# Optimization experiments

Hardware: AMD Instinct MI355X
Metric: run time of the kernel (lower is better)

The kernel has to match this reference:

```python
import jax, jax.numpy as jnp
import numpy as np

N_CHANNELS = 8
SECTION = 32768
F_IN = 64
F_OUT = 64
UNITS = 512


def setup_inputs() -> dict:
    key = jax.random.key(0)
    ks = jax.random.split(key, 10)
    scale = lambda fan_in: 1.0 / np.sqrt(fan_in)
    return {
        "x": jax.random.normal(ks[0], (N_CHANNELS * SECTION, F_IN), jnp.float32),
        "w0": jax.random.normal(ks[1], (N_CHANNELS, UNITS, F_IN), jnp.float32) * scale(F_IN),
        "w1": jax.random.normal(ks[2], (N_CHANNELS, UNITS, UNITS), jnp.float32) * scale(UNITS),
        "w2": jax.random.normal(ks[3], (N_CHANNELS, UNITS, UNITS), jnp.float32) * scale(UNITS),
        "w3": jax.random.normal(ks[4], (N_CHANNELS, F_OUT, UNITS), jnp.float32) * scale(UNITS),
        "b0": jax.random.normal(ks[5], (N_CHANNELS, UNITS), jnp.float32) * 0.01,
        "b1": jax.random.normal(ks[6], (N_CHANNELS, UNITS), jnp.float32) * 0.01,
        "b2": jax.random.normal(ks[7], (N_CHANNELS, UNITS), jnp.float32) * 0.01,
        "b3": jax.random.normal(ks[8], (N_CHANNELS, F_OUT), jnp.float32) * 0.01,
        "section_size": SECTION,
    }


def reference(x, w0, w1, w2, w3, b0, b1, b2, b3, section_size):
    # Equal sections of size `section_size` per channel: reshape to [C, S, F]
    # and run the per-channel MLP as batched (grouped) GEMMs.
    C = w0.shape[0]
    xs = x.reshape(C, section_size, -1)  # [C, S, F_in]
    for w, b in ((w0, b0), (w1, b1), (w2, b2)):
        xs = jax.nn.relu(jnp.einsum('csi,coi->cso', xs, w) + b[:, None, :])
    ys = jnp.einsum('csi,coi->cso', xs, w3) + b3[:, None, :]  # [C, S, F_out]
    return ys.reshape(C * section_size, -1)
```

## Files before the change

### kernel.cpp

```cpp
#include <hip/hip_runtime.h>
#include <hip/hip_bf16.h>

#define CH 8
#define SEC 32768
#define FIN 64
#define FOUT 64
#define UN 512
#define BM 64

typedef __bf16 bf16;
typedef bf16 bf16x8 __attribute__((ext_vector_type(8)));
typedef bf16 bf16x4 __attribute__((ext_vector_type(4)));
typedef float f32x4 __attribute__((ext_vector_type(4)));

__device__ __forceinline__ bf16x8 cvt8(const float* __restrict__ src) {
  f32x4 u0 = *(const f32x4*)src;
  f32x4 u1 = *(const f32x4*)(src + 4);
  bf16x8 v;
  v[0] = (bf16)u0[0]; v[1] = (bf16)u0[1]; v[2] = (bf16)u0[2]; v[3] = (bf16)u0[3];
  v[4] = (bf16)u1[0]; v[5] = (bf16)u1[1]; v[6] = (bf16)u1[2]; v[7] = (bf16)u1[3];
  return v;
}

__device__ __forceinline__ void store_cvt8(void* dst, const float* __restrict__ src) {
  *(bf16x8*)dst = cvt8(src);
}

template<int K, bool WSPATH>
__device__ __forceinline__ void run_main_layer(
    const bf16* __restrict__ wb,
    const float* __restrict__ wf,
    const float* __restrict__ bias, char* __restrict__ act,
    int w, int l, int l15, int l4, int rot)
{
  constexpr int NKS = K / 32;
  constexpr int MASK = NKS - 1;
  const int col0 = w * 64;
  const char* abase = act + l * 16;

  f32x4 acc[4][4];
#pragma unroll
  for (int mt = 0; mt < 4; ++mt)
#pragma unroll
    for (int nt = 0; nt < 4; ++nt)
      acc[mt][nt] = f32x4{0.f, 0.f, 0.f, 0.f};

  if constexpr (WSPATH) {
    const bf16* bp = wb + ((size_t)(w * 4) * NKS * 64 + l) * 8;

    bf16x8 B0[4], B1[4];
    {
      const int ks0 = rot & MASK;
#pragma unroll
      for (int i = 0; i < 4; ++i)
        B0[i] = *(const bf16x8*)(bp + ((size_t)i * NKS + ks0) * 512);
    }

#pragma unroll
    for (int j = 0; j < NKS; j += 2) {
      {
        const int ksn = (j + 1 + rot) & MASK;
#pragma unroll
        for (int i = 0; i < 4; ++i)
          B1[i] = *(const bf16x8*)(bp + ((size_t)i * NKS + ksn) * 512);
        const int ks = (j + rot) & MASK;
        bf16x8 a[4];
#pragma unroll
        for (int mt = 0; mt < 4; ++mt)
          a[mt] = *(const bf16x8*)(abase + (mt * NKS + ks) * 1024);
        __builtin_amdgcn_s_setprio(1);
#pragma unroll
        for (int mt = 0; mt < 4; ++mt)
#pragma unroll
          for (int nt = 0; nt < 4; ++nt)
            acc[mt][nt] = __builtin_amdgcn_mfma_f32_16x16x32_bf16(a[mt], B0[nt], acc[mt][nt], 0, 0, 0);
        __builtin_amdgcn_s_setprio(0);
      }
      {
        if (j + 2 < NKS) {
          const int ksn = (j + 2 + rot) & MASK;
#pragma unroll
          for (int i = 0; i < 4; ++i)
            B0[i] = *(const bf16x8*)(bp + ((size_t)i * NKS + ksn) * 512);
        }
        const int ks = (j + 1 + rot) & MASK;
        bf16x8 a[4];
#pragma unroll
        for (int mt = 0; mt < 4; ++mt)
          a[mt] = *(const bf16x8*)(abase + (mt * NKS + ks) * 1024);
        __builtin_amdgcn_s_setprio(1);
#pragma unroll
        for (int mt = 0; mt < 4; ++mt)
#pragma unroll
          for (int nt = 0; nt < 4; ++nt)
            acc[mt][nt] = __builtin_amdgcn_mfma_f32_16x16x32_bf16(a[mt], B1[nt], acc[mt][nt], 0, 0, 0);
        __builtin_amdgcn_s_setprio(0);
      }
    }
  } else {
    const float* bpf[4];
#pragma unroll
    for (int nt = 0; nt < 4; ++nt)
      bpf[nt] = wf + (size_t)(col0 + nt * 16 + l15) * K + l4 * 8;
    for (int j = 0; j < NKS; ++j) {
      const int ks = (j + rot) & MASK;
      bf16x8 a[4], b[4];
#pragma unroll
      for (int nt = 0; nt < 4; ++nt) b[nt] = cvt8(bpf[nt] + ks * 32);
#pragma unroll
      for (int mt = 0; mt < 4; ++mt)
        a[mt] = *(const bf16x8*)(abase + (mt * NKS + ks) * 1024);
#pragma unroll
      for (int mt = 0; mt < 4; ++mt)
#pragma unroll
        for (int nt = 0; nt < 4; ++nt)
          acc[mt][nt] = __builtin_amdgcn_mfma_f32_16x16x32_bf16(a[mt], b[nt], acc[mt][nt], 0, 0, 0);
    }
  }

  __syncthreads();

#pragma unroll
  for (int nt = 0; nt < 4; ++nt) {
    const int col = col0 + nt * 16 + l15;
    const float bv = bias[col];
    const int base = (col >> 5) * 1024 + ((col >> 3) & 3) * 256 + (col & 7) * 2 + l4 * 64;
#pragma unroll
    for (int mt = 0; mt < 4; ++mt)
#pragma unroll
      for (int r = 0; r < 4; ++r) {
        float v = acc[mt][nt][r] + bv;
        v = v > 0.f ? v : 0.f;
        *(bf16*)(act + mt * 16384 + base + r * 16) = (bf16)v;
      }
  }
  __syncthreads();
}

template<bool WSPATH>
__device__ __forceinline__ void run_final_layer(
    const bf16* __restrict__ wb, const float* __restrict__ wf,
    const float* __restrict__ bias, const char* __restrict__ act,
    float* __restrict__ gout,
    int w, int l, int l15, int l4, int rot)
{
  constexpr int NKS = 16;
  const int mt = w >> 1;
  const int nb = (w & 1) * 2;
  const char* abase = act + mt * 16384 + l * 16;

  f32x4 acc[2];
  acc[0] = f32x4{0.f, 0.f, 0.f, 0.f};
  acc[1] = f32x4{0.f, 0.f, 0.f, 0.f};

  if constexpr (WSPATH) {
    const bf16* bp0 = wb + ((size_t)(nb + 0) * 16 * 64 + l) * 8;
    const bf16* bp1 = wb + ((size_t)(nb + 1) * 16 * 64 + l) * 8;
    bf16x8 B0[2], B1[2];
    B0[0] = *(const bf16x8*)(bp0 + (size_t)(rot & 15) * 512);
    B0[1] = *(const bf16x8*)(bp1 + (size_t)(rot & 15) * 512);
#pragma unroll
    for (int j = 0; j < NKS; j += 2) {
      {
        const int ksn = (j + 1 + rot) & 15;
        B1[0] = *(const bf16x8*)(bp0 + (size_t)ksn * 512);
        B1[1] = *(const bf16x8*)(bp1 + (size_t)ksn * 512);
        const int ks = (j + rot) & 15;
        const bf16x8 a = *(const bf16x8*)(abase + ks * 1024);
        acc[0] = __builtin_amdgcn_mfma_f32_16x16x32_bf16(a, B0[0], acc[0], 0, 0, 0);
        acc[1] = __builtin_amdgcn_mfma_f32_16x16x32_bf16(a, B0[1], acc[1], 0, 0, 0);
      }
      {
        if (j + 2 < NKS) {
          const int ksn = (j + 2 + rot) & 15;
          B0[0] = *(const bf16x8*)(bp0 + (size_t)ksn * 512);
          B0[1] = *(const bf16x8*)(bp1 + (size_t)ksn * 512);
        }
        const int ks = (j + 1 + rot) & 15;
        const bf16x8 a = *(const bf16x8*)(abase + ks * 1024);
        acc[0] = __builtin_amdgcn_mfma_f32_16x16x32_bf16(a, B1[0], acc[0], 0, 0, 0);
        acc[1] = __builtin_amdgcn_mfma_f32_16x16x32_bf16(a, B1[1], acc[1], 0, 0, 0);
      }
    }
  } else {
    const float* bpf0 = wf + (size_t)((nb + 0) * 16 + l15) * UN + l4 * 8;
    const float* bpf1 = wf + (size_t)((nb + 1) * 16 + l15) * UN + l4 * 8;
    for (int j = 0; j < NKS; ++j) {
      const int ks = (j + rot) & 15;
      const bf16x8 b0 = cvt8(bpf0 + ks * 32);
      const bf16x8 b1 = cvt8(bpf1 + ks * 32);
      const bf16x8 a = *(const bf16x8*)(abase + ks * 1024);
      acc[0] = __builtin_amdgcn_mfma_f32_16x16x32_bf16(a, b0, acc[0], 0, 0, 0);
      acc[1] = __builtin_amdgcn_mfma_f32_16x16x32_bf16(a, b1, acc[1], 0, 0, 0);
    }
  }

#pragma unroll
  for (int i = 0; i < 2; ++i) {
    const int col = (nb + i) * 16 + l15;
    const float bv = bias[col];
#pragma unroll
    for (int r = 0; r < 4; ++r)
      gout[(size_t)(mt * 16 + l4 * 4 + r) * FOUT + col] = acc[i][r] + bv;
  }
}

template<bool WSPATH>
__global__ __launch_bounds__(512, 2) void mlp_fused(
    const float* __restrict__ x,
    const float* __restrict__ w0f, const float* __restrict__ w1f,
    const float* __restrict__ w2f, const float* __restrict__ w3f,
    const float* __restrict__ b0, const float* __restrict__ b1,
    const float* __restrict__ b2, const float* __restrict__ b3,
    const bf16* __restrict__ wbase,
    float* __restrict__ out)
{
  extern __shared__ char smem[];
  char* act = smem;

  const int tid = threadIdx.x;
  const int w = tid >> 6, l = tid & 63;
  const int l15 = l & 15, l4 = l >> 4;

  const int wg = (blockIdx.x & 7) * 512 + (blockIdx.x >> 3);
  const int ch = wg >> 9;
  const int row0 = (wg & 511) * BM;
  const int rot = wg & 15;

  const bf16* w0b = wbase + (size_t)ch * UN * FIN;
  const bf16* w1b = wbase + CH * UN * FIN + (size_t)ch * UN * UN;
  const bf16* w2b = wbase + CH * UN * FIN + CH * UN * UN + (size_t)ch * UN * UN;
  const bf16* w3b = wbase + CH * UN * FIN + 2 * CH * UN * UN + (size_t)ch * FOUT * UN;
  const float* w0c = w0f + (size_t)ch * UN * FIN;
  const float* w1c = w1f + (size_t)ch * UN * UN;
  const float* w2c = w2f + (size_t)ch * UN * UN;
  const float* w3c = w3f + (size_t)ch * FOUT * UN;
  const float* b0c = b0 + ch * UN;
  const float* b1c = b1 + ch * UN;
  const float* b2c = b2 + ch * UN;
  const float* b3c = b3 + ch * FOUT;

  {
    const float* xs = x + (size_t)(ch * SEC + row0) * FIN;
    store_cvt8(act + w * 1024 + l * 16,
               xs + ((w >> 1) * 16 + l15) * FIN + (w & 1) * 32 + l4 * 8);
  }
  __syncthreads();

  run_main_layer<64,  WSPATH>(w0b, w0c, b0c, act, w, l, l15, l4, rot);
  run_main_layer<512, WSPATH>(w1b, w1c, b1c, act, w, l, l15, l4, rot);
  run_main_layer<512, WSPATH>(w2b, w2c, b2c, act, w, l, l15, l4, rot);
  run_final_layer<WSPATH>(w3b, w3c, b3c, act,
                          out + (size_t)(ch * SEC + row0) * FOUT,
                          w, l, l15, l4, rot);
}

template<int K, int N>
__device__ __forceinline__ void cvt_one(const float* __restrict__ src,
                                        bf16* __restrict__ dst, int t)
{
  constexpr int NKS = K / 32;
  constexpr int perCh = N * K / 8;
  const int ch = t / perCh;
  const int r = t - ch * perCh;
  const int l = r & 63;
  const int p = r >> 6;
  const int ks = p & (NKS - 1);
  const int f = p / NKS;
  const float* s = src + (size_t)ch * N * K + (size_t)(f * 16 + (l & 15)) * K
                 + ks * 32 + (l >> 4) * 8;
  store_cvt8(dst + (size_t)t * 8, s);
}

__global__ void cvt_weights(const float* __restrict__ w0, const float* __restrict__ w1,
                            const float* __restrict__ w2, const float* __restrict__ w3,
                            bf16* __restrict__ o)
{
  constexpr int T0 = CH * UN * FIN / 8;
  constexpr int T1 = CH * UN * UN / 8;
  constexpr int total = 2 * T0 + 2 * T1;
  for (int t = blockIdx.x * blockDim.x + threadIdx.x; t < total;
       t += gridDim.x * blockDim.x) {
    if (t < T0)                cvt_one<FIN, UN>(w0, o, t);
    else if (t < T0 + T1)      cvt_one<UN, UN>(w1, o + CH * UN * FIN, t - T0);
    else if (t < T0 + 2 * T1)  cvt_one<UN, UN>(w2, o + CH * UN * FIN + CH * UN * UN, t - T0 - T1);
    else                       cvt_one<UN, FOUT>(w3, o + CH * UN * FIN + 2 * CH * UN * UN, t - T0 - 2 * T1);
  }
}

extern "C" void kernel_launch(void* const* d_in, const int* in_sizes, int n_in,
                              void* d_out, int out_size, void* d_ws, size_t ws_size,
                              hipStream_t stream)
{
  const float* x  = (const float*)d_in[0];
  const float* w0 = (const float*)d_in[1];
  const float* w1 = (const float*)d_in[2];
  const float* w2 = (const float*)d_in[3];
  const float* w3 = (const float*)d_in[4];
  const float* b0 = (const float*)d_in[5];
  const float* b1 = (const float*)d_in[6];
  const float* b2 = (const float*)d_in[7];
  const float* b3 = (const float*)d_in[8];
  float* out = (float*)d_out;

  const int grid = CH * (SEC / BM);
  const size_t wbytes = (size_t)(2 * CH * UN * FIN + 2 * CH * UN * UN) * 2;

  if (ws_size >= wbytes) {
    bf16* wb = (bf16*)d_ws;
    hipLaunchKernelGGL(cvt_weights, dim3(2304), dim3(256), 0, stream, w0, w1, w2, w3, wb);
    hipFuncSetAttribute(reinterpret_cast<const void*>(mlp_fused<true>),
                        hipFuncAttributeMaxDynamicSharedMemorySize, 65536);
    hipLaunchKernelGGL(mlp_fused<true>, dim3(grid), dim3(512), 65536, stream,
                       x, w0, w1, w2, w3, b0, b1, b2, b3, wb, out);
  } else {
    hipFuncSetAttribute(reinterpret_cast<const void*>(mlp_fused<false>),
                        hipFuncAttributeMaxDynamicSharedMemorySize, 65536);
    hipLaunchKernelGGL(mlp_fused<false>, dim3(grid), dim3(512), 65536, stream,
                       x, w0, w1, w2, w3, b0, b1, b2, b3, (const bf16*)nullptr, out);
  }
}
```

Measured before the change: 309.5 us.

## Swap MFMA operands to emit transposed tiles with packed bf16x4 stores, drop K rotation

Swaps the A/B operands of every MFMA so each lane holds four consecutive output columns for one row. The epilogue can then load the bias as a float4, pack four bf16 results into one 8-byte LDS store, and write the final fp32 output with 16-byte global stores instead of scalar ones. It also removes the per-workgroup K-start rotation, which makes all loop offsets compile-time constants, and fully unrolls the fallback path. The aim is fewer LDS and global store instructions and simpler addressing. Without the rotation, workgroups on the same channel may read the same weight lines at the same time.

Result: faster. 302.8 us (-2.1%).

```diff
diff --git a/kernel.cpp b/kernel.cpp
--- a/kernel.cpp
+++ b/kernel.cpp
@@ -31,10 +31,9 @@
     const bf16* __restrict__ wb,
     const float* __restrict__ wf,
     const float* __restrict__ bias, char* __restrict__ act,
-    int w, int l, int l15, int l4, int rot)
+    int w, int l, int l15, int l4)
 {
   constexpr int NKS = K / 32;
-  constexpr int MASK = NKS - 1;
   const int col0 = w * 64;
   const char* abase = act + l * 16;
 
@@ -47,53 +46,47 @@
 
   if constexpr (WSPATH) {
     const bf16* bp = wb + ((size_t)(w * 4) * NKS * 64 + l) * 8;
-
     bf16x8 B0[4], B1[4];
-    {
-      const int ks0 = rot & MASK;
-#pragma unroll
-      for (int i = 0; i < 4; ++i)
-        B0[i] = *(const bf16x8*)(bp + ((size_t)i * NKS + ks0) * 512);
-    }
+#pragma unroll
+    for (int i = 0; i < 4; ++i)
+      B0[i] = *(const bf16x8*)(bp + (size_t)(i * NKS) * 512);
 
 #pragma unroll
     for (int j = 0; j < NKS; j += 2) {
+      if (j + 1 < NKS) {
+#pragma unroll
+        for (int i = 0; i < 4; ++i)
+          B1[i] = *(const bf16x8*)(bp + (size_t)(i * NKS + j + 1) * 512);
+      }
       {
-        const int ksn = (j + 1 + rot) & MASK;
+        bf16x8 a[4];
+#pragma unroll
+        for (int mt = 0; mt < 4; ++mt)
+          a[mt] = *(const bf16x8*)(abase + (mt * NKS + j) * 1024);
+        __builtin_amdgcn_s_setprio(1);
+#pragma unroll
+        for (int mt = 0; mt < 4; ++mt)
+#pragma unroll
+          for (int nt = 0; nt < 4; ++nt)
+            acc[mt][nt] = __builtin_amdgcn_mfma_f32_16x16x32_bf16(B0[nt], a[mt], acc[mt][nt], 0, 0, 0);
+        __builtin_amdgcn_s_setprio(0);
+      }
+      if (j + 2 < NKS) {
 #pragma unroll
         for (int i = 0; i < 4; ++i)
-          B1[i] = *(const bf16x8*)(bp + ((size_t)i * NKS + ksn) * 512);
-        const int ks = (j + rot) & MASK;
+          B0[i] = *(const bf16x8*)(bp + (size_t)(i * NKS + j + 2) * 512);
+      }
+      if (j + 1 < NKS) {
         bf16x8 a[4];
 #pragma unroll
         for (int mt = 0; mt < 4; ++mt)
-          a[mt] = *(const bf16x8*)(abase + (mt * NKS + ks) * 1024);
+          a[mt] = *(const bf16x8*)(abase + (mt * NKS + j + 1) * 1024);
         __builtin_amdgcn_s_setprio(1);
 #pragma unroll
         for (int mt = 0; mt < 4; ++mt)
 #pragma unroll
           for (int nt = 0; nt < 4; ++nt)
-            acc[mt][nt] = __builtin_amdgcn_mfma_f32_16x16x32_bf16(a[mt], B0[nt], acc[mt][nt], 0, 0, 0);
-        __builtin_amdgcn_s_setprio(0);
-      }
-      {
-        if (j + 2 < NKS) {
-          const int ksn = (j + 2 + rot) & MASK;
-#pragma unroll
-          for (int i = 0; i < 4; ++i)
-            B0[i] = *(const bf16x8*)(bp + ((size_t)i * NKS + ksn) * 512);
-        }
-        const int ks = (j + 1 + rot) & MASK;
-        bf16x8 a[4];
-#pragma unroll
-        for (int mt = 0; mt < 4; ++mt)
-          a[mt] = *(const bf16x8*)(abase + (mt * NKS + ks) * 1024);
-        __builtin_amdgcn_s_setprio(1);
-#pragma unroll
-        for (int mt = 0; mt < 4; ++mt)
-#pragma unroll
-          for (int nt = 0; nt < 4; ++nt)
-            acc[mt][nt] = __builtin_amdgcn_mfma_f32_16x16x32_bf16(a[mt], B1[nt], acc[mt][nt], 0, 0, 0);
+            acc[mt][nt] = __builtin_amdgcn_mfma_f32_16x16x32_bf16(B1[nt], a[mt], acc[mt][nt], 0, 0, 0);
         __builtin_amdgcn_s_setprio(0);
       }
     }
@@ -102,19 +95,19 @@
 #pragma unroll
     for (int nt = 0; nt < 4; ++nt)
       bpf[nt] = wf + (size_t)(col0 + nt * 16 + l15) * K + l4 * 8;
+#pragma unroll
     for (int j = 0; j < NKS; ++j) {
-      const int ks = (j + rot) & MASK;
       bf16x8 a[4], b[4];
 #pragma unroll
-      for (int nt = 0; nt < 4; ++nt) b[nt] = cvt8(bpf[nt] + ks * 32);
+      for (int nt = 0; nt < 4; ++nt) b[nt] = cvt8(bpf[nt] + j * 32);
 #pragma unroll
       for (int mt = 0; mt < 4; ++mt)
-        a[mt] = *(const bf16x8*)(abase + (mt * NKS + ks) * 1024);
+        a[mt] = *(const bf16x8*)(abase + (mt * NKS + j) * 1024);
 #pragma unroll
       for (int mt = 0; mt < 4; ++mt)
 #pragma unroll
         for (int nt = 0; nt < 4; ++nt)
-          acc[mt][nt] = __builtin_amdgcn_mfma_f32_16x16x32_bf16(a[mt], b[nt], acc[mt][nt], 0, 0, 0);
+          acc[mt][nt] = __builtin_amdgcn_mfma_f32_16x16x32_bf16(b[nt], a[mt], acc[mt][nt], 0, 0, 0);
     }
   }
 
@@ -122,17 +115,20 @@
 
 #pragma unroll
   for (int nt = 0; nt < 4; ++nt) {
-    const int col = col0 + nt * 16 + l15;
-    const float bv = bias[col];
-    const int base = (col >> 5) * 1024 + ((col >> 3) & 3) * 256 + (col & 7) * 2 + l4 * 64;
-#pragma unroll
-    for (int mt = 0; mt < 4; ++mt)
+    const f32x4 bv = *(const f32x4*)(bias + col0 + nt * 16 + l4 * 4);
+    const int slot = l15 + ((nt & 1) * 2 + (l4 >> 1)) * 16;
+    const int ksp  = w * 2 + (nt >> 1);
+    const int boff = slot * 16 + (l4 & 1) * 8;
+#pragma unroll
+    for (int mt = 0; mt < 4; ++mt) {
+      bf16x4 pk;
 #pragma unroll
       for (int r = 0; r < 4; ++r) {
-        float v = acc[mt][nt][r] + bv;
-        v = v > 0.f ? v : 0.f;
-        *(bf16*)(act + mt * 16384 + base + r * 16) = (bf16)v;
-      }
+        const float v = acc[mt][nt][r] + bv[r];
+        pk[r] = (bf16)(v > 0.f ? v : 0.f);
+      }
+      *(bf16x4*)(act + (mt * 16 + ksp) * 1024 + boff) = pk;
+    }
   }
   __syncthreads();
 }
@@ -142,7 +138,7 @@
     const bf16* __restrict__ wb, const float* __restrict__ wf,
     const float* __restrict__ bias, const char* __restrict__ act,
     float* __restrict__ gout,
-    int w, int l, int l15, int l4, int rot)
+    int w, int l, int l15, int l4)
 {
   constexpr int NKS = 16;
   const int mt = w >> 1;
@@ -157,51 +153,47 @@
     const bf16* bp0 = wb + ((size_t)(nb + 0) * 16 * 64 + l) * 8;
     const bf16* bp1 = wb + ((size_t)(nb + 1) * 16 * 64 + l) * 8;
     bf16x8 B0[2], B1[2];
-    B0[0] = *(const bf16x8*)(bp0 + (size_t)(rot & 15) * 512);
-    B0[1] = *(const bf16x8*)(bp1 + (size_t)(rot & 15) * 512);
+    B0[0] = *(const bf16x8*)(bp0);
+    B0[1] = *(const bf16x8*)(bp1);
 #pragma unroll
     for (int j = 0; j < NKS; j += 2) {
       {
-        const int ksn = (j + 1 + rot) & 15;
-        B1[0] = *(const bf16x8*)(bp0 + (size_t)ksn * 512);
-        B1[1] = *(const bf16x8*)(bp1 + (size_t)ksn * 512);
-        const int ks = (j + rot) & 15;
-        const bf16x8 a = *(const bf16x8*)(abase + ks * 1024);
-        acc[0] = __builtin_amdgcn_mfma_f32_16x16x32_bf16(a, B0[0], acc[0], 0, 0, 0);
-        acc[1] = __builtin_amdgcn_mfma_f32_16x16x32_bf16(a, B0[1], acc[1], 0, 0, 0);
+        B1[0] = *(const bf16x8*)(bp0 + (size_t)(j + 1) * 512);
+        B1[1] = *(const bf16x8*)(bp1 + (size_t)(j + 1) * 512);
+        const bf16x8 a = *(const bf16x8*)(abase + j * 1024);
+        acc[0] = __builtin_amdgcn_mfma_f32_16x16x32_bf16(B0[0], a, acc[0], 0, 0, 0);
+        acc[1] = __builtin_amdgcn_mfma_f32_16x16x32_bf16(B0[1], a, acc[1], 0, 0, 0);
       }
       {
         if (j + 2 < NKS) {
-          const int ksn = (j + 2 + rot) & 15;
-          B0[0] = *(const bf16x8*)(bp0 + (size_t)ksn * 512);
-          B0[1] = *(const bf16x8*)(bp1 + (size_t)ksn * 512);
+          B0[0] = *(const bf16x8*)(bp0 + (size_t)(j + 2) * 512);
+          B0[1] = *(const bf16x8*)(bp1 + (size_t)(j + 2) * 512);
         }
-        const int ks = (j + 1 + rot) & 15;
-        const bf16x8 a = *(const bf16x8*)(abase + ks * 1024);
-        acc[0] = __builtin_amdgcn_mfma_f32_16x16x32_bf16(a, B1[0], acc[0], 0, 0, 0);
-        acc[1] = __builtin_amdgcn_mfma_f32_16x16x32_bf16(a, B1[1], acc[1], 0, 0, 0);
+        const bf16x8 a = *(const bf16x8*)(abase + (j + 1) * 1024);
+        acc[0] = __builtin_amdgcn_mfma_f32_16x16x32_bf16(B1[0], a, acc[0], 0, 0, 0);
+        acc[1] = __builtin_amdgcn_mfma_f32_16x16x32_bf16(B1[1], a, acc[1], 0, 0, 0);
       }
     }
   } else {
     const float* bpf0 = wf + (size_t)((nb + 0) * 16 + l15) * UN + l4 * 8;
     const float* bpf1 = wf + (size_t)((nb + 1) * 16 + l15) * UN + l4 * 8;
+#pragma unroll
     for (int j = 0; j < NKS; ++j) {
-      const int ks = (j + rot) & 15;
-      const bf16x8 b0 = cvt8(bpf0 + ks * 32);
-      const bf16x8 b1 = cvt8(bpf1 + ks * 32);
-      const bf16x8 a = *(const bf16x8*)(abase + ks * 1024);
-      acc[0] = __builtin_amdgcn_mfma_f32_16x16x32_bf16(a, b0, acc[0], 0, 0, 0);
-      acc[1] = __builtin_amdgcn_mfma_f32_16x16x32_bf16(a, b1, acc[1], 0, 0, 0);
+      const bf16x8 b0 = cvt8(bpf0 + j * 32);
+      const bf16x8 b1 = cvt8(bpf1 + j * 32);
+      const bf16x8 a = *(const bf16x8*)(abase + j * 1024);
+      acc[0] = __builtin_amdgcn_mfma_f32_16x16x32_bf16(b0, a, acc[0], 0, 0, 0);
+      acc[1] = __builtin_amdgcn_mfma_f32_16x16x32_bf16(b1, a, acc[1], 0, 0, 0);
     }
   }
 
 #pragma unroll
   for (int i = 0; i < 2; ++i) {
-    const int col = (nb + i) * 16 + l15;
-    const float bv = bias[col];
-#pragma unroll
-    for (int r = 0; r < 4; ++r)
-      gout[(size_t)(mt * 16 + l4 * 4 + r) * FOUT + col] = acc[i][r] + bv;
+    const f32x4 bv = *(const f32x4*)(bias + (nb + i) * 16 + l4 * 4);
+    f32x4 o;
+#pragma unroll
+    for (int r = 0; r < 4; ++r) o[r] = acc[i][r] + bv[r];
+    *(f32x4*)(gout + (size_t)(mt * 16 + l15) * FOUT + (nb + i) * 16 + l4 * 4) = o;
   }
 }
 
@@ -225,7 +217,6 @@
   const int wg = (blockIdx.x & 7) * 512 + (blockIdx.x >> 3);
   const int ch = wg >> 9;
   const int row0 = (wg & 511) * BM;
-  const int rot = wg & 15;
 
   const bf16* w0b = wbase + (size_t)ch * UN * FIN;
   const bf16* w1b = wbase + CH * UN * FIN + (size_t)ch * UN * UN;
@@ -247,12 +238,12 @@
   }
   __syncthreads();
 
-  run_main_layer<64,  WSPATH>(w0b, w0c, b0c, act, w, l, l15, l4, rot);
-  run_main_layer<512, WSPATH>(w1b, w1c, b1c, act, w, l, l15, l4, rot);
-  run_main_layer<512, WSPATH>(w2b, w2c, b2c, act, w, l, l15, l4, rot);
+  run_main_layer<64,  WSPATH>(w0b, w0c, b0c, act, w, l, l15, l4);
+  run_main_layer<512, WSPATH>(w1b, w1c, b1c, act, w, l, l15, l4);
+  run_main_layer<512, WSPATH>(w2b, w2c, b2c, act, w, l, l15, l4);
   run_final_layer<WSPATH>(w3b, w3c, b3c, act,
                           out + (size_t)(ch * SEC + row0) * FOUT,
-                          w, l, l15, l4, rot);
+                          w, l, l15, l4);
 }
 
 template<int K, int N>
```
